# Performance work log

Measured on AMD Instinct MI355X. Metric: run time of the kernel, lower is better.

The kernel has to match this reference:

```python
import jax, jax.numpy as jnp
import numpy as np

KEY_DIM = 32
NUM_HEADS = 4
B, T, F, D = 32, 64, 128, 64


def _proj_in(x, w, b):
    # x: [B,T,F,D], w: [D,H,K], b: [H,K] -> [B,T,F,H,K]
    return jnp.einsum("btfd,dhk->btfhk", x, w) + b


def _axial_mha(x, wq, bq, wk, bk, wv, bv, wo, bo, axis):
    # Keras MultiHeadAttention with attention_axes=(axis,); dropout inactive at inference.
    scale = 1.0 / np.sqrt(KEY_DIM)
    q = _proj_in(x, wq, bq) * scale
    k = _proj_in(x, wk, bk)
    v = _proj_in(x, wv, bv)
    if axis == 1:  # temporal attention, feature axis acts as batch
        scores = jnp.einsum("bqfhk,bsfhk->bfhqs", q, k)  # [B,F,H,Tq,Tk]
        probs = jax.nn.softmax(scores, axis=-1)
        o = jnp.einsum("bfhqs,bsfhk->bqfhk", probs, v)
    else:  # feature attention, temporal axis acts as batch
        scores = jnp.einsum("btqhk,btshk->bthqs", q, k)  # [B,T,H,Fq,Fk]
        probs = jax.nn.softmax(scores, axis=-1)
        o = jnp.einsum("bthqs,btshk->btqhk", probs, v)
    return jnp.einsum("btfhk,hkd->btfd", o, wo) + bo


def setup_inputs() -> dict:
    key = jax.random.key(0)
    ks = jax.random.split(key, 10)
    std = 0.02
    w = lambda k, shape: (jax.random.normal(k, shape, jnp.float32) * std)
    inp = {"x": jax.random.normal(ks[0], (B, T, F, D), jnp.float32)}
    for i, n in enumerate(["tq", "tk", "tv", "fq", "fk", "fv"]):
        inp[n + "_w"] = w(ks[1 + i], (D, NUM_HEADS, KEY_DIM))
        inp[n + "_b"] = jnp.zeros((NUM_HEADS, KEY_DIM), jnp.float32)
    inp["to_w"] = w(ks[7], (NUM_HEADS, KEY_DIM, D))
    inp["to_b"] = jnp.zeros((D,), jnp.float32)
    inp["fo_w"] = w(ks[8], (NUM_HEADS, KEY_DIM, D))
    inp["fo_b"] = jnp.zeros((D,), jnp.float32)
    return inp


def reference(x, tq_w, tq_b, tk_w, tk_b, tv_w, tv_b, to_w, to_b,
              fq_w, fq_b, fk_w, fk_b, fv_w, fv_b, fo_w, fo_b):
    temporal_out = _axial_mha(x, tq_w, tq_b, tk_w, tk_b, tv_w, tv_b, to_w, to_b, axis=1)
    feature_out = _axial_mha(x, fq_w, fq_b, fk_w, fk_b, fv_w, fv_b, fo_w, fo_b, axis=2)
    return temporal_out + feature_out
```

## Files before the change

### kernel.cpp

```cpp
#include <hip/hip_runtime.h>

typedef unsigned short u16;
typedef unsigned int   u32;
typedef short v8s __attribute__((ext_vector_type(8)));
typedef float v4f __attribute__((ext_vector_type(4)));
typedef u32   v4u __attribute__((ext_vector_type(4)));

#define DEV __device__ __forceinline__
#define MFMA(a,b,c) __builtin_amdgcn_mfma_f32_16x16x32_bf16((a),(b),(c),0,0,0)

constexpr int Bb = 32, Tt = 64, Ff = 128, Dd = 64, Hh = 4, Kk = 32;

DEV u16 f2b(float f) {
    u32 u = __float_as_uint(f);
    return (u16)((u + 0x7fffu + ((u >> 16) & 1u)) >> 16);
}
DEV u32 pk2(float a, float b) {
    u32 r;
    asm("v_cvt_pk_bf16_f32 %0, %1, %2" : "=v"(r) : "v"(a), "v"(b));
    return r;
}

DEV v8s redist(u32 lo0, u32 hi0, u32 lo1, u32 hi1, int sA, int sB, int hiHalf) {
    int aL0 = __shfl((int)lo0, sA), aH0 = __shfl((int)hi0, sA);
    int aL1 = __shfl((int)lo1, sA), aH1 = __shfl((int)hi1, sA);
    int bL0 = __shfl((int)lo0, sB), bH0 = __shfl((int)hi0, sB);
    int bL1 = __shfl((int)lo1, sB), bH1 = __shfl((int)hi1, sB);
    v4u r;
    r[0] = (u32)(hiHalf ? aL1 : aL0);
    r[1] = (u32)(hiHalf ? aH1 : aH0);
    r[2] = (u32)(hiHalf ? bL1 : bL0);
    r[3] = (u32)(hiHalf ? bH1 : bH0);
    union { v4u u; v8s s; } c; c.u = r;
    return c.s;
}

__global__ __launch_bounds__(256)
void prep_weights(const float* __restrict__ tq, const float* __restrict__ tk,
                  const float* __restrict__ tv, const float* __restrict__ fq,
                  const float* __restrict__ fk, const float* __restrict__ fv,
                  const float* __restrict__ to_, const float* __restrict__ fo,
                  u16* __restrict__ ws)
{
    int idx = blockIdx.x * 256 + threadIdx.x;
    if (idx < 49152) {
        int p = idx >> 13, rem = idx & 8191;
        int h = rem >> 11, ch = (rem >> 6) & 31, d = rem & 63;
        const float* w = (p==0)?tq:(p==1)?tk:(p==2)?tv:(p==3)?fq:(p==4)?fk:fv;
        ws[idx] = f2b(w[d*128 + h*32 + ch]);
    } else {
        int i2 = idx - 49152;
        int path = i2 >> 13, rem = i2 & 8191;
        int h = rem >> 11, d = (rem >> 5) & 63, k2 = rem & 31;
        const float* w = path ? fo : to_;
        ws[idx] = f2b(w[h*2048 + k2*64 + d]);
    }
}

template<int NR, int MODE>
__global__ __launch_bounds__(NR*4)
void axial_mfma(const float* __restrict__ x, const u16* __restrict__ wsw,
                const float* __restrict__ bq, const float* __restrict__ bk,
                const float* __restrict__ bv, const float* __restrict__ bo,
                float* __restrict__ out)
{
    constexpr int W   = NR / 16;
    constexpr int QP  = 40;
    constexpr int NRp = NR + 8;
    constexpr int BUF = NR * QP + 32 * NRp;
    constexpr int SMEM = 2 * BUF;
    __shared__ alignas(16) u16 sm[SMEM];

    const int tid  = threadIdx.x;
    const int w    = tid >> 6;
    const int lane = tid & 63;
    const int quad = lane >> 4;
    const int l15  = lane & 15;
    const int bid  = blockIdx.x;

    const int sA = ((quad & 1) << 5) | l15;
    const int sB = sA + 16;
    const int hiH = quad >> 1;

    int base, rstride;
    if (MODE == 0) { int b = bid >> 7, f = bid & 127; base = b*(Tt*Ff*Dd) + f*Dd; rstride = Ff*Dd; }
    else           { base = bid * (Ff*Dd); rstride = Dd; }

    constexpr int PB = (MODE == 0) ? 0 : 3;
    const u16* wql = wsw + (PB+0)*8192;
    const u16* wkl = wsw + (PB+1)*8192;
    const u16* wvl = wsw + (PB+2)*8192;
    const u16* wol = wsw + 49152 + MODE*8192;

    v8s xfrag[2];
#pragma unroll
    for (int ks = 0; ks < 2; ++ks) {
        const float* xp = x + base + (w*16 + l15)*rstride + ks*32 + quad*8;
        float4 a = *reinterpret_cast<const float4*>(xp);
        float4 b = *reinterpret_cast<const float4*>(xp + 4);
        v8s f;
        u32* fu = reinterpret_cast<u32*>(&f);
        fu[0] = pk2(a.x, a.y); fu[1] = pk2(a.z, a.w);
        fu[2] = pk2(b.x, b.y); fu[3] = pk2(b.z, b.w);
        xfrag[ks] = f;
    }

    v4f outAcc[4];
#pragma unroll
    for (int i = 0; i < 4; ++i) outAcc[i] = (v4f){0.f,0.f,0.f,0.f};

    const float scale = 0.17677669529663687f;
    const v4f vzero = (v4f){0.f,0.f,0.f,0.f};

#pragma unroll 1
    for (int h = 0; h < Hh; ++h) {
        const int bb   = (h & 1) * BUF;
        const int o_k  = bb;
        const int o_vt = bb + NR * QP;

        u32 qlo[2], qhi[2];
        {
            const u16* wb = wql + h*2048;
#pragma unroll
            for (int nt = 0; nt < 2; ++nt) {
                v4f acc = vzero;
#pragma unroll
                for (int ks = 0; ks < 2; ++ks) {
                    v8s wf = *reinterpret_cast<const v8s*>(wb + (nt*16+l15)*64 + ks*32 + quad*8);
                    acc = MFMA(wf, xfrag[ks], acc);
                }
                float4 b4 = *reinterpret_cast<const float4*>(bq + h*32 + nt*16 + quad*4);
                qlo[nt] = pk2((acc[0]+b4.x)*scale, (acc[1]+b4.y)*scale);
                qhi[nt] = pk2((acc[2]+b4.z)*scale, (acc[3]+b4.w)*scale);
            }
        }
        v8s qf = redist(qlo[0], qhi[0], qlo[1], qhi[1], sA, sB, hiH);

        {
            const u16* wb = wkl + h*2048;
#pragma unroll
            for (int nt = 0; nt < 2; ++nt) {
                v4f acc = vzero;
#pragma unroll
                for (int ks = 0; ks < 2; ++ks) {
                    v8s wf = *reinterpret_cast<const v8s*>(wb + (nt*16+l15)*64 + ks*32 + quad*8);
                    acc = MFMA(wf, xfrag[ks], acc);
                }
                float4 b4 = *reinterpret_cast<const float4*>(bk + h*32 + nt*16 + quad*4);
                u32 lo = pk2(acc[0]+b4.x, acc[1]+b4.y);
                u32 hi = pk2(acc[2]+b4.z, acc[3]+b4.w);
                *reinterpret_cast<uint2*>(&sm[o_k + (w*16+l15)*QP + nt*16 + quad*4]) = make_uint2(lo, hi);
            }
        }
        {
            const u16* wb = wvl + h*2048;
#pragma unroll
            for (int nt = 0; nt < 2; ++nt) {
                v4f acc = vzero;
#pragma unroll
                for (int ks = 0; ks < 2; ++ks) {
                    v8s wf = *reinterpret_cast<const v8s*>(wb + (nt*16+l15)*64 + ks*32 + quad*8);
                    acc = MFMA(xfrag[ks], wf, acc);
                }
                float bias = bv[h*32 + nt*16 + l15];
                u32 lo = pk2(acc[0]+bias, acc[1]+bias);
                u32 hi = pk2(acc[2]+bias, acc[3]+bias);
                int ch = nt*16 + l15;
                *reinterpret_cast<uint2*>(&sm[o_vt + ch*NRp + w*16 + quad*4]) = make_uint2(lo, hi);
            }
        }
        __syncthreads();

        v4f S[W];
#pragma unroll
        for (int ct = 0; ct < W; ++ct) {
            v8s kf = *reinterpret_cast<const v8s*>(&sm[o_k + (ct*16+l15)*QP + quad*8]);
            S[ct] = MFMA(kf, qf, vzero);
        }
        float cm[W];
#pragma unroll
        for (int ct = 0; ct < W; ++ct)
            cm[ct] = fmaxf(fmaxf(S[ct][0], S[ct][1]), fmaxf(S[ct][2], S[ct][3]));
        float mm = cm[0];
#pragma unroll
        for (int ct = 1; ct < W; ++ct) mm = fmaxf(mm, cm[ct]);
        mm = fmaxf(mm, __shfl_xor(mm, 16));
        mm = fmaxf(mm, __shfl_xor(mm, 32));
        float ss = 0.f;
        u32 pl[2*W];
#pragma unroll
        for (int ct = 0; ct < W; ++ct) {
            float p0 = __expf(S[ct][0] - mm), p1 = __expf(S[ct][1] - mm);
            float p2 = __expf(S[ct][2] - mm), p3 = __expf(S[ct][3] - mm);
            ss += (p0 + p1) + (p2 + p3);
            pl[2*ct  ] = pk2(p0, p1);
            pl[2*ct+1] = pk2(p2, p3);
        }
        ss += __shfl_xor(ss, 16);
        ss += __shfl_xor(ss, 32);
        float rl = 1.f / ss;

        v4f Oacc[2] = { vzero, vzero };
#pragma unroll
        for (int ks = 0; ks < NR/32; ++ks) {
            v8s pf = redist(pl[4*ks], pl[4*ks+1], pl[4*ks+2], pl[4*ks+3], sA, sB, hiH);
#pragma unroll
            for (int nt = 0; nt < 2; ++nt) {
                v8s vf = *reinterpret_cast<const v8s*>(&sm[o_vt + (nt*16+l15)*NRp + ks*32 + quad*8]);
                Oacc[nt] = MFMA(vf, pf, Oacc[nt]);
            }
        }
        u32 olo[2], ohi[2];
#pragma unroll
        for (int nt = 0; nt < 2; ++nt) {
            olo[nt] = pk2(Oacc[nt][0]*rl, Oacc[nt][1]*rl);
            ohi[nt] = pk2(Oacc[nt][2]*rl, Oacc[nt][3]*rl);
        }
        v8s of = redist(olo[0], ohi[0], olo[1], ohi[1], sA, sB, hiH);

        {
            const u16* wb = wol + h*2048;
#pragma unroll
            for (int nt = 0; nt < 4; ++nt) {
                v8s wf = *reinterpret_cast<const v8s*>(wb + (nt*16+l15)*32 + quad*8);
                outAcc[nt] = MFMA(wf, of, outAcc[nt]);
            }
        }
    }

    float* orow = out + base + (w*16 + l15)*rstride;
#pragma unroll
    for (int nt = 0; nt < 4; ++nt) {
        int d0 = nt*16 + quad*4;
        float4 b4 = *reinterpret_cast<const float4*>(bo + d0);
        float4 v = make_float4(outAcc[nt][0]+b4.x, outAcc[nt][1]+b4.y,
                               outAcc[nt][2]+b4.z, outAcc[nt][3]+b4.w);
        if (MODE == 1) {
            float4 p = *reinterpret_cast<const float4*>(orow + d0);
            v.x += p.x; v.y += p.y; v.z += p.z; v.w += p.w;
        }
        *reinterpret_cast<float4*>(orow + d0) = v;
    }
}

extern "C" void kernel_launch(void* const* d_in, const int* in_sizes, int n_in,
                              void* d_out, int out_size, void* d_ws, size_t ws_size,
                              hipStream_t stream) {
    const float* x   = (const float*)d_in[0];
    const float* tqw = (const float*)d_in[1];  const float* tqb = (const float*)d_in[2];
    const float* tkw = (const float*)d_in[3];  const float* tkb = (const float*)d_in[4];
    const float* tvw = (const float*)d_in[5];  const float* tvb = (const float*)d_in[6];
    const float* fqw = (const float*)d_in[7];  const float* fqb = (const float*)d_in[8];
    const float* fkw = (const float*)d_in[9];  const float* fkb = (const float*)d_in[10];
    const float* fvw = (const float*)d_in[11]; const float* fvb = (const float*)d_in[12];
    const float* tow = (const float*)d_in[13]; const float* tob = (const float*)d_in[14];
    const float* fow = (const float*)d_in[15]; const float* fob = (const float*)d_in[16];
    float* out = (float*)d_out;
    u16* ws = (u16*)d_ws;

    hipLaunchKernelGGL(prep_weights, dim3(256), dim3(256), 0, stream,
                       tqw, tkw, tvw, fqw, fkw, fvw, tow, fow, ws);
    hipLaunchKernelGGL((axial_mfma<64,0>), dim3(Bb*Ff), dim3(256), 0, stream,
                       x, ws, tqb, tkb, tvb, tob, out);
    hipLaunchKernelGGL((axial_mfma<128,1>), dim3(Bb*Tt), dim3(512), 0, stream,
                       x, ws, fqb, fkb, fvb, fob, out);
}
```

Baseline: 384.4 us.

## Replace temporal attention kernel with single-wave register-resident kernel split by query half

Adds a new temporal attention kernel in which one 64-lane wave handles half of the query rows for one (batch, feature) column. All Q/K/V projections, softmax, PV and output projection stay in registers, with cross-lane shuffles (redist) in place of LDS staging. The aim is to drop shared memory traffic and block-level synchronisation and to launch twice as many small blocks for better occupancy. In exchange, each of the two half-blocks recomputes K and V for the full sequence, and weight fragments are read directly from global memory with no LDS reuse.

```diff
diff --git a/kernel.cpp b/kernel.cpp
--- a/kernel.cpp
+++ b/kernel.cpp
@@ -57,6 +57,187 @@
     }
 }
 
+__global__ __launch_bounds__(64)
+void temporal_wave(const float* __restrict__ x, const u16* __restrict__ wsw,
+                   const float* __restrict__ bq, const float* __restrict__ bk,
+                   const float* __restrict__ bv, const float* __restrict__ bo,
+                   float* __restrict__ out)
+{
+    const int lane = threadIdx.x;
+    const int quad = lane >> 4;
+    const int l15  = lane & 15;
+    const int bid  = blockIdx.x;
+    const int rh   = bid >> 12;
+    const int bf   = bid & 4095;
+    const int b    = bf >> 7, f = bf & 127;
+    const int base = b*(Tt*Ff*Dd) + f*Dd;
+    constexpr int rstride = Ff*Dd;
+
+    const int sA = ((quad & 1) << 5) | l15;
+    const int sB = sA + 16;
+    const int hiH = quad >> 1;
+
+    const u16* wql = wsw + 0*8192;
+    const u16* wkl = wsw + 1*8192;
+    const u16* wvl = wsw + 2*8192;
+    const u16* wol = wsw + 49152;
+
+    v8s xf[4][2];
+#pragma unroll
+    for (int kt = 0; kt < 4; ++kt)
+#pragma unroll
+        for (int ks = 0; ks < 2; ++ks) {
+            const float* xp = x + base + (kt*16 + l15)*rstride + ks*32 + quad*8;
+            float4 a = *reinterpret_cast<const float4*>(xp);
+            float4 c = *reinterpret_cast<const float4*>(xp + 4);
+            v8s fr;
+            u32* fu = reinterpret_cast<u32*>(&fr);
+            fu[0] = pk2(a.x, a.y); fu[1] = pk2(a.z, a.w);
+            fu[2] = pk2(c.x, c.y); fu[3] = pk2(c.z, c.w);
+            xf[kt][ks] = fr;
+        }
+
+    v8s xq_[2][2];
+#pragma unroll
+    for (int qt = 0; qt < 2; ++qt)
+#pragma unroll
+        for (int ks = 0; ks < 2; ++ks)
+            xq_[qt][ks] = rh ? xf[2+qt][ks] : xf[qt][ks];
+
+    v4f outAcc[2][4];
+#pragma unroll
+    for (int i = 0; i < 2; ++i)
+#pragma unroll
+        for (int j = 0; j < 4; ++j) outAcc[i][j] = (v4f){0.f,0.f,0.f,0.f};
+
+    const float scale = 0.17677669529663687f;
+    const v4f vzero = (v4f){0.f,0.f,0.f,0.f};
+
+#pragma unroll 1
+    for (int h = 0; h < Hh; ++h) {
+        v8s kf[4];
+#pragma unroll
+        for (int kt = 0; kt < 4; ++kt) {
+            u32 lo[2], hi[2];
+#pragma unroll
+            for (int nt = 0; nt < 2; ++nt) {
+                v4f acc = vzero;
+#pragma unroll
+                for (int ks = 0; ks < 2; ++ks) {
+                    v8s wf = *reinterpret_cast<const v8s*>(wkl + h*2048 + (nt*16+l15)*64 + ks*32 + quad*8);
+                    acc = MFMA(wf, xf[kt][ks], acc);
+                }
+                float4 b4 = *reinterpret_cast<const float4*>(bk + h*32 + nt*16 + quad*4);
+                lo[nt] = pk2(acc[0]+b4.x, acc[1]+b4.y);
+                hi[nt] = pk2(acc[2]+b4.z, acc[3]+b4.w);
+            }
+            kf[kt] = redist(lo[0], hi[0], lo[1], hi[1], sA, sB, hiH);
+        }
+
+        u32 vlo[4][2], vhi[4][2];
+#pragma unroll
+        for (int kt = 0; kt < 4; ++kt)
+#pragma unroll
+            for (int nt = 0; nt < 2; ++nt) {
+                v4f acc = vzero;
+#pragma unroll
+                for (int ks = 0; ks < 2; ++ks) {
+                    v8s wf = *reinterpret_cast<const v8s*>(wvl + h*2048 + (nt*16+l15)*64 + ks*32 + quad*8);
+                    acc = MFMA(xf[kt][ks], wf, acc);
+                }
+                float bias = bv[h*32 + nt*16 + l15];
+                vlo[kt][nt] = pk2(acc[0]+bias, acc[1]+bias);
+                vhi[kt][nt] = pk2(acc[2]+bias, acc[3]+bias);
+            }
+        v8s vf[2][2];
+#pragma unroll
+        for (int w2 = 0; w2 < 2; ++w2)
+#pragma unroll
+            for (int nt = 0; nt < 2; ++nt)
+                vf[w2][nt] = redist(vlo[2*w2][nt], vhi[2*w2][nt],
+                                    vlo[2*w2+1][nt], vhi[2*w2+1][nt], sA, sB, hiH);
+
+#pragma unroll
+        for (int qt = 0; qt < 2; ++qt) {
+            u32 qlo[2], qhi[2];
+#pragma unroll
+            for (int nt = 0; nt < 2; ++nt) {
+                v4f acc = vzero;
+#pragma unroll
+                for (int ks = 0; ks < 2; ++ks) {
+                    v8s wf = *reinterpret_cast<const v8s*>(wql + h*2048 + (nt*16+l15)*64 + ks*32 + quad*8);
+                    acc = MFMA(wf, xq_[qt][ks], acc);
+                }
+                float4 b4 = *reinterpret_cast<const float4*>(bq + h*32 + nt*16 + quad*4);
+                qlo[nt] = pk2((acc[0]+b4.x)*scale, (acc[1]+b4.y)*scale);
+                qhi[nt] = pk2((acc[2]+b4.z)*scale, (acc[3]+b4.w)*scale);
+            }
+            v8s qf = redist(qlo[0], qhi[0], qlo[1], qhi[1], sA, sB, hiH);
+
+            v4f S[4];
+#pragma unroll
+            for (int kt = 0; kt < 4; ++kt)
+                S[kt] = MFMA(kf[kt], qf, vzero);
+
+            float cm[4];
+#pragma unroll
+            for (int kt = 0; kt < 4; ++kt)
+                cm[kt] = fmaxf(fmaxf(S[kt][0], S[kt][1]), fmaxf(S[kt][2], S[kt][3]));
+            float mm = fmaxf(fmaxf(cm[0], cm[1]), fmaxf(cm[2], cm[3]));
+            mm = fmaxf(mm, __shfl_xor(mm, 16));
+            mm = fmaxf(mm, __shfl_xor(mm, 32));
+            float ss = 0.f;
+            u32 pl[8];
+#pragma unroll
+            for (int kt = 0; kt < 4; ++kt) {
+                float p0 = __expf(S[kt][0] - mm), p1 = __expf(S[kt][1] - mm);
+                float p2 = __expf(S[kt][2] - mm), p3 = __expf(S[kt][3] - mm);
+                ss += (p0 + p1) + (p2 + p3);
+                pl[2*kt  ] = pk2(p0, p1);
+                pl[2*kt+1] = pk2(p2, p3);
+            }
+            ss += __shfl_xor(ss, 16);
+            ss += __shfl_xor(ss, 32);
+            float rl = 1.f / ss;
+
+            v4f Oacc[2] = { vzero, vzero };
+#pragma unroll
+            for (int w2 = 0; w2 < 2; ++w2) {
+                v8s pf = redist(pl[4*w2], pl[4*w2+1], pl[4*w2+2], pl[4*w2+3], sA, sB, hiH);
+#pragma unroll
+                for (int nt = 0; nt < 2; ++nt)
+                    Oacc[nt] = MFMA(vf[w2][nt], pf, Oacc[nt]);
+            }
+            u32 olo[2], ohi[2];
+#pragma unroll
+            for (int nt = 0; nt < 2; ++nt) {
+                olo[nt] = pk2(Oacc[nt][0]*rl, Oacc[nt][1]*rl);
+                ohi[nt] = pk2(Oacc[nt][2]*rl, Oacc[nt][3]*rl);
+            }
+            v8s of = redist(olo[0], ohi[0], olo[1], ohi[1], sA, sB, hiH);
+
+#pragma unroll
+            for (int nt = 0; nt < 4; ++nt) {
+                v8s wf = *reinterpret_cast<const v8s*>(wol + h*2048 + (nt*16+l15)*32 + quad*8);
+                outAcc[qt][nt] = MFMA(wf, of, outAcc[qt][nt]);
+            }
+        }
+    }
+
+#pragma unroll
+    for (int qt = 0; qt < 2; ++qt) {
+        float* orow = out + base + (rh*32 + qt*16 + l15)*rstride;
+#pragma unroll
+        for (int nt = 0; nt < 4; ++nt) {
+            int d0 = nt*16 + quad*4;
+            float4 b4 = *reinterpret_cast<const float4*>(bo + d0);
+            float4 v = make_float4(outAcc[qt][nt][0]+b4.x, outAcc[qt][nt][1]+b4.y,
+                                   outAcc[qt][nt][2]+b4.z, outAcc[qt][nt][3]+b4.w);
+            *reinterpret_cast<float4*>(orow + d0) = v;
+        }
+    }
+}
+
 template<int NR, int MODE>
 __global__ __launch_bounds__(NR*4)
 void axial_mfma(const float* __restrict__ x, const u16* __restrict__ wsw,
@@ -260,7 +441,7 @@
 
     hipLaunchKernelGGL(prep_weights, dim3(256), dim3(256), 0, stream,
                        tqw, tkw, tvw, fqw, fkw, fvw, tow, fow, ws);
-    hipLaunchKernelGGL((axial_mfma<64,0>), dim3(Bb*Ff), dim3(256), 0, stream,
+    hipLaunchKernelGGL(temporal_wave, dim3(2*Bb*Ff), dim3(64), 0, stream,
                        x, ws, tqb, tkb, tvb, tob, out);
     hipLaunchKernelGGL((axial_mfma<128,1>), dim3(Bb*Tt), dim3(512), 0, stream,
                        x, ws, fqb, fkb, fvb, fob, out);
```

New measurement: 354.3 us (median of 3 runs). 1.08x faster.
